# Performance work log

Hardware: AMD Instinct MI355X
Metric: run time of the kernel (lower is better)

The kernel has to match this reference:

```python
import jax, jax.numpy as jnp
import numpy as np

N, E, G = 4096, 16384, 16
IN_C, EDGE_C, H = 3, 4, 128
LN_EPS = 1e-5


def setup_inputs() -> dict:
    key = jax.random.key(0)
    ks = jax.random.split(key, 32)
    nrm = lambda k, shp, s: jax.random.normal(k, shp, jnp.float32) * s
    inp = {}
    inp["x"] = nrm(ks[0], (N, IN_C), 1.0)
    inp["edge_index"] = jax.random.randint(ks[1], (2, E), 0, N)
    inp["edge_attr"] = nrm(ks[2], (E, EDGE_C), 1.0)
    inp["batch"] = jnp.sort(jax.random.randint(ks[3], (N,), 0, G))
    inp["contingency_type"] = nrm(ks[4], (G, 4), 1.0)
    inp["load_scale"] = nrm(ks[5], (G,), 1.0)
    i = 6
    def conv_params(prefix, in_c):
        nonlocal i
        inp[prefix + "_w1"] = nrm(ks[i], (EDGE_C, 128), 1.0 / np.sqrt(EDGE_C)); i += 1
        inp[prefix + "_b1"] = jnp.zeros((128,), jnp.float32)
        inp[prefix + "_w2"] = nrm(ks[i], (128, in_c * H), 1.0 / np.sqrt(128)); i += 1
        inp[prefix + "_b2"] = jnp.zeros((in_c * H,), jnp.float32)
        inp[prefix + "_root"] = nrm(ks[i], (in_c, H), 1.0 / np.sqrt(in_c)); i += 1
        inp[prefix + "_bias"] = jnp.zeros((H,), jnp.float32)
    conv_params("c1", IN_C)
    conv_params("c2", H)
    conv_params("c3", H)
    for p in ("ln1", "ln2", "ln3"):
        inp[p + "_g"] = jnp.ones((H,), jnp.float32)
        inp[p + "_b"] = jnp.zeros((H,), jnp.float32)
    inp["lin_w"] = nrm(ks[i], (2 * H + 4 + 1, 2), 1.0 / np.sqrt(2 * H + 5)); i += 1
    inp["lin_b"] = jnp.zeros((2,), jnp.float32)
    return inp


def _nnconv(x, src, dst, edge_attr, w1, b1, w2, b2, root, bias, in_c):
    # edge MLP -> per-edge weight matrix [E, in_c, H]
    h = jax.nn.relu(edge_attr @ w1 + b1)
    W = (h @ w2 + b2).reshape(-1, in_c, H)
    msg = jnp.einsum('ei,eio->eo', x[src], W)  # gather + per-edge matmul
    s = jax.ops.segment_sum(msg, dst, num_segments=N)
    cnt = jax.ops.segment_sum(jnp.ones((msg.shape[0],), msg.dtype), dst, num_segments=N)
    agg = s / jnp.maximum(cnt, 1.0)[:, None]  # scatter-mean
    return agg + x @ root + bias


def _layernorm(x, g, b):
    m = jnp.mean(x, axis=-1, keepdims=True)
    v = jnp.mean(jnp.square(x - m), axis=-1, keepdims=True)
    return (x - m) * jax.lax.rsqrt(v + LN_EPS) * g + b


def reference(x, edge_index, edge_attr, batch, contingency_type, load_scale,
              c1_w1, c1_b1, c1_w2, c1_b2, c1_root, c1_bias,
              c2_w1, c2_b1, c2_w2, c2_b2, c2_root, c2_bias,
              c3_w1, c3_b1, c3_w2, c3_b2, c3_root, c3_bias,
              ln1_g, ln1_b, ln2_g, ln2_b, ln3_g, ln3_b,
              lin_w, lin_b):
    src, dst = edge_index[0], edge_index[1]
    h = _nnconv(x, src, dst, edge_attr, c1_w1, c1_b1, c1_w2, c1_b2, c1_root, c1_bias, IN_C)
    h = jax.nn.relu(_layernorm(h, ln1_g, ln1_b))
    h = _nnconv(h, src, dst, edge_attr, c2_w1, c2_b1, c2_w2, c2_b2, c2_root, c2_bias, H)
    h = jax.nn.elu(_layernorm(h, ln2_g, ln2_b))
    h = _nnconv(h, src, dst, edge_attr, c3_w1, c3_b1, c3_w2, c3_b2, c3_root, c3_bias, H)
    h = jax.nn.leaky_relu(_layernorm(h, ln3_g, ln3_b), negative_slope=0.01)
    # global mean / max pool over graphs
    gsum = jax.ops.segment_sum(h, batch, num_segments=G)
    gcnt = jax.ops.segment_sum(jnp.ones((N,), h.dtype), batch, num_segments=G)
    gmean = gsum / jnp.maximum(gcnt, 1.0)[:, None]
    gmax = jax.ops.segment_max(h, batch, num_segments=G)
    gmax = jnp.where(gcnt[:, None] > 0, gmax, 0.0)
    x_cat = jnp.concatenate([gmean, gmax, contingency_type, load_scale[:, None]], axis=1)
    return x_cat @ lin_w + lin_b
```

## Files before the change

### kernel.cpp

```cpp
#include <hip/hip_runtime.h>
#include <hip/hip_bf16.h>


#define N_NODES 4096
#define N_EDGES 16384
#define N_GRAPHS 16
#define HD 128
#define BM 128
#define LDB 136
#define KSPLIT 2
#define KT_PER (HD / KSPLIT)
#define SLAB_E (HD * HD)
#define PN 32

typedef unsigned short ushort_t;
typedef __attribute__((ext_vector_type(8))) short short8;
typedef __attribute__((ext_vector_type(4))) float f32x4;

static __device__ __forceinline__ ushort_t f2b(float f) {
    __hip_bfloat16 h = __float2bfloat16(f);
    union { __hip_bfloat16 h; ushort_t u; } cv; cv.h = h; return cv.u;
}
static __device__ __forceinline__ float b2f(ushort_t u) {
    union { unsigned u; float f; } cv; cv.u = ((unsigned)u) << 16; return cv.f;
}

static __device__ __forceinline__ float wave_sum(float v) {
#pragma unroll
    for (int off = 1; off < 64; off <<= 1) v += __shfl_xor(v, off, 64);
    return v;
}

__global__ __launch_bounds__(256) void count_k(const int* __restrict__ dst, float* __restrict__ cnt) {
    int e = blockIdx.x * 256 + threadIdx.x;
    atomicAdd(&cnt[dst[e]], 1.0f);
}

__global__ __launch_bounds__(128) void l1_edge(
    const float* __restrict__ x, const int* __restrict__ src, const int* __restrict__ dst,
    const float* __restrict__ ea, const float* __restrict__ w1, const float* __restrict__ b1,
    const float* __restrict__ w2, const float* __restrict__ b2, float* __restrict__ agg) {
    __shared__ float h[4][HD];
    __shared__ float xsrc[4][3];
    const int o = threadIdx.x;
    const int e0 = blockIdx.x * 4;
#pragma unroll
    for (int q = 0; q < 4; ++q) {
        float s = b1[o];
#pragma unroll
        for (int j = 0; j < 4; ++j) s = fmaf(ea[(e0 + q) * 4 + j], w1[j * HD + o], s);
        h[q][o] = fmaxf(s, 0.0f);
    }
    if (o < 12) { int q = o / 3, i = o % 3; xsrc[q][i] = x[src[e0 + q] * 3 + i]; }
    __syncthreads();
    float acc[4] = {0.f, 0.f, 0.f, 0.f};
    for (int i = 0; i < 3; ++i) {
        float bb = b2[i * HD + o];
        float w[4] = {bb, bb, bb, bb};
        for (int k = 0; k < HD; ++k) {
            float w2v = w2[k * 384 + i * HD + o];
#pragma unroll
            for (int q = 0; q < 4; ++q) w[q] = fmaf(h[q][k], w2v, w[q]);
        }
#pragma unroll
        for (int q = 0; q < 4; ++q) acc[q] = fmaf(xsrc[q][i], w[q], acc[q]);
    }
#pragma unroll
    for (int q = 0; q < 4; ++q) atomicAdd(&agg[dst[e0 + q] * HD + o], acc[q]);
}

__global__ __launch_bounds__(128) void node_update_l1(
    float* __restrict__ agg, const float* __restrict__ cnt, const float* __restrict__ x,
    const float* __restrict__ root, const float* __restrict__ bias,
    const float* __restrict__ lng, const float* __restrict__ lnb) {
    const int n = blockIdx.x, o = threadIdx.x;
    float s = bias[o];
#pragma unroll
    for (int i = 0; i < 3; ++i) s = fmaf(x[n * 3 + i], root[i * HD + o], s);
    float v = agg[n * HD + o] / fmaxf(cnt[n], 1.0f) + s;
    __shared__ float red[2];
    float ws = wave_sum(v);
    if ((o & 63) == 0) red[o >> 6] = ws;
    __syncthreads();
    float m = (red[0] + red[1]) * (1.0f / HD);
    float d = v - m;
    float ws2 = wave_sum(d * d);
    __syncthreads();
    if ((o & 63) == 0) red[o >> 6] = ws2;
    __syncthreads();
    float var = (red[0] + red[1]) * (1.0f / HD);
    float y = d * rsqrtf(var + 1e-5f) * lng[o] + lnb[o];
    agg[n * HD + o] = fmaxf(y, 0.0f);
}

__global__ __launch_bounds__(256) void w2t_prep(const float* __restrict__ w2,
                                                const float* __restrict__ b2,
                                                ushort_t* __restrict__ w2t) {
    __shared__ ushort_t tile[HD][LDB];
    const int kt = blockIdx.x;
    const int t = threadIdx.x;
    const float* srcp = (kt < HD) ? (w2 + kt * HD * HD) : b2;
    for (int c = 0; c < 64; ++c) {
        int flat = c * 256 + t;
        int i = flat >> 7, o = flat & 127;
        tile[o][i] = f2b(srcp[i * HD + o]);
    }
    __syncthreads();
    uint4* outp = (uint4*)(w2t + (size_t)kt * SLAB_E);
    for (int it = 0; it < 8; ++it) {
        int c = it * 256 + t;
        int ng = c >> 9, j = (c >> 6) & 7, l = c & 63;
        int ni = j >> 2, kb = j & 3;
        int R  = ng * 32 + ni * 16 + (l & 15);
        int ke = kb * 32 + (l >> 4) * 8;
        outp[c] = *(const uint4*)&tile[R][ke];
    }
}

__global__ __launch_bounds__(512, 2) void gemm_mfma(
    const float* __restrict__ hprev, const float* __restrict__ ea,
    const float* __restrict__ w1, const float* __restrict__ b1,
    const ushort_t* __restrict__ w2t,
    const int* __restrict__ src, const int* __restrict__ dst,
    float* __restrict__ agg) {
    __shared__ ushort_t Xs[SLAB_E];
    __shared__ ushort_t HeT[KT_PER][BM];

    const int t = threadIdx.x;
    const int lane = t & 63, quad = lane >> 4, l16 = lane & 15;
    const int wave = t >> 6;
    const int mg = wave >> 2;
    const int ng = wave & 3;
    const int eb = blockIdx.x >> 1;
    const int ks = blockIdx.x & 1;
    const int k0 = ks * KT_PER;
    const int e0 = eb * BM;
    const int rbase = mg * 64;

    {
        const int le = t >> 2;
        const int j0 = (t & 3) * 4;
        const int r7 = le & 7;
        const float* rp = hprev + src[e0 + le] * HD + (t & 3) * 32;
        ushort_t* xrow = Xs + le * HD;
#pragma unroll
        for (int c = 0; c < 4; ++c) {
            float4 va = ((const float4*)rp)[2 * c];
            float4 vb = ((const float4*)rp)[2 * c + 1];
            uint4 pk;
            pk.x = (unsigned)f2b(va.x) | ((unsigned)f2b(va.y) << 16);
            pk.y = (unsigned)f2b(va.z) | ((unsigned)f2b(va.w) << 16);
            pk.z = (unsigned)f2b(vb.x) | ((unsigned)f2b(vb.y) << 16);
            pk.w = (unsigned)f2b(vb.z) | ((unsigned)f2b(vb.w) << 16);
            *(uint4*)&xrow[((j0 + c) ^ r7) << 3] = pk;
        }
    }

    {
        const int e = t & 127;
        const float4 av = ((const float4*)ea)[e0 + e];
        for (int kl = t >> 7; kl < KT_PER; kl += 4) {
            const int kt = k0 + kl;
            float s = b1[kt];
            s = fmaf(av.x, w1[0 * HD + kt], s);
            s = fmaf(av.y, w1[1 * HD + kt], s);
            s = fmaf(av.z, w1[2 * HD + kt], s);
            s = fmaf(av.w, w1[3 * HD + kt], s);
            HeT[kl][e] = f2b(fmaxf(s, 0.0f));
        }
    }
    __syncthreads();

    short8 afrag[4][4];
#pragma unroll
    for (int mi = 0; mi < 4; ++mi) {
        const int R = rbase + mi * 16 + l16;
        const ushort_t* rowp = Xs + R * HD;
        const int r7 = R & 7;
#pragma unroll
        for (int kb = 0; kb < 4; ++kb)
            afrag[mi][kb] = *(const short8*)&rowp[((kb * 4 + quad) ^ r7) << 3];
    }

    f32x4 acc[4][2];
#pragma unroll
    for (int mi = 0; mi < 4; ++mi)
#pragma unroll
        for (int ni = 0; ni < 2; ++ni)
            acc[mi][ni] = (f32x4){0.f, 0.f, 0.f, 0.f};

    const ushort_t* bbase = w2t + (size_t)ng * 4096 + (size_t)lane * 8;

#define LOADB(bf, slab)                                                         \
    {                                                                           \
        const ushort_t* bw = bbase + (size_t)(slab) * SLAB_E;                   \
        _Pragma("unroll") for (int ni = 0; ni < 2; ++ni)                        \
            _Pragma("unroll") for (int kb = 0; kb < 4; ++kb)                    \
                bf[ni][kb] = *(const short8*)(bw + (ni * 4 + kb) * 512);        \
    }
#define CONSUME(bf, s)                                                          \
    {                                                                           \
        _Pragma("unroll") for (int mi = 0; mi < 4; ++mi) {                      \
            ushort4 hv = *(const ushort4*)&HeT[s][rbase + mi * 16 + quad * 4];  \
            float h0 = b2f(hv.x), h1 = b2f(hv.y), h2 = b2f(hv.z), h3 = b2f(hv.w);\
            _Pragma("unroll") for (int ni = 0; ni < 2; ++ni) {                  \
                f32x4 p = {0.f, 0.f, 0.f, 0.f};                                 \
                _Pragma("unroll") for (int kb = 0; kb < 4; ++kb)                \
                    p = __builtin_amdgcn_mfma_f32_16x16x32_bf16(                \
                        afrag[mi][kb], bf[ni][kb], p, 0, 0, 0);                 \
                acc[mi][ni][0] = fmaf(h0, p[0], acc[mi][ni][0]);                \
                acc[mi][ni][1] = fmaf(h1, p[1], acc[mi][ni][1]);                \
                acc[mi][ni][2] = fmaf(h2, p[2], acc[mi][ni][2]);                \
                acc[mi][ni][3] = fmaf(h3, p[3], acc[mi][ni][3]);                \
            }                                                                   \
        }                                                                       \
    }

    short8 bfA[2][4], bfB[2][4];
    LOADB(bfA, k0);
    for (int s = 0; s < KT_PER; s += 2) {
        LOADB(bfB, k0 + s + 1);
        CONSUME(bfA, s);
        __builtin_amdgcn_s_barrier();
        if (s + 2 < KT_PER) LOADB(bfA, k0 + s + 2)
        else if (ks == 1)   LOADB(bfA, HD);
        CONSUME(bfB, s + 1);
        __builtin_amdgcn_s_barrier();
    }
    if (ks == 1) {
#pragma unroll
        for (int mi = 0; mi < 4; ++mi)
#pragma unroll
            for (int ni = 0; ni < 2; ++ni) {
                f32x4 p = {0.f, 0.f, 0.f, 0.f};
#pragma unroll
                for (int kb = 0; kb < 4; ++kb)
                    p = __builtin_amdgcn_mfma_f32_16x16x32_bf16(
                        afrag[mi][kb], bfA[ni][kb], p, 0, 0, 0);
                acc[mi][ni][0] += p[0]; acc[mi][ni][1] += p[1];
                acc[mi][ni][2] += p[2]; acc[mi][ni][3] += p[3];
            }
    }
#undef LOADB
#undef CONSUME

#pragma unroll
    for (int mi = 0; mi < 4; ++mi) {
#pragma unroll
        for (int r = 0; r < 4; ++r) {
            const int dn = dst[e0 + rbase + mi * 16 + quad * 4 + r];
#pragma unroll
            for (int ni = 0; ni < 2; ++ni)
                atomicAdd(&agg[dn * HD + ng * 32 + ni * 16 + l16], acc[mi][ni][r]);
        }
    }
}

__global__ __launch_bounds__(128) void node_update(
    float* __restrict__ agg, const float* __restrict__ cnt,
    const float* __restrict__ hprev, const float* __restrict__ root, const float* __restrict__ bias,
    const float* __restrict__ lng, const float* __restrict__ lnb, int act) {
    const int n = blockIdx.x, o = threadIdx.x;
    __shared__ float hr[HD];
    hr[o] = hprev[n * HD + o];
    __syncthreads();
    float s = bias[o];
#pragma unroll 8
    for (int k = 0; k < HD; ++k) s = fmaf(hr[k], root[k * HD + o], s);
    float v = agg[n * HD + o] / fmaxf(cnt[n], 1.0f) + s;
    __shared__ float red[2];
    float ws = wave_sum(v);
    if ((o & 63) == 0) red[o >> 6] = ws;
    __syncthreads();
    float m = (red[0] + red[1]) * (1.0f / HD);
    float d = v - m;
    float ws2 = wave_sum(d * d);
    __syncthreads();
    if ((o & 63) == 0) red[o >> 6] = ws2;
    __syncthreads();
    float var = (red[0] + red[1]) * (1.0f / HD);
    float y = d * rsqrtf(var + 1e-5f) * lng[o] + lnb[o];
    if (act == 1) y = (y > 0.0f) ? y : expm1f(y);
    else y = (y > 0.0f) ? y : 0.01f * y;
    agg[n * HD + o] = y;
}

static __device__ __forceinline__ unsigned fkey(float f) {
    unsigned b = __float_as_uint(f);
    return (b & 0x80000000u) ? ~b : (b | 0x80000000u);
}
__global__ __launch_bounds__(128) void pool_scatter(
    const float* __restrict__ h3, const int* __restrict__ batch,
    float* __restrict__ gsum, unsigned* __restrict__ gmaxk, int* __restrict__ gcnt) {
    const int o = threadIdx.x;
    const int nb = blockIdx.x * PN;
    float sum = 0.0f, mx = -3.0e38f;
    int gcur = batch[nb];
    int run = 0;
    for (int j = 0; j < PN; ++j) {
        const int n = nb + j;
        const int g = batch[n];
        const float v = h3[n * HD + o];
        if (g != gcur) {
            atomicAdd(&gsum[gcur * HD + o], sum);
            atomicMax(&gmaxk[gcur * HD + o], fkey(mx));
            if (o == 0) atomicAdd(&gcnt[gcur], run);
            sum = 0.0f; mx = -3.0e38f; run = 0; gcur = g;
        }
        sum += v; mx = fmaxf(mx, v); ++run;
    }
    atomicAdd(&gsum[gcur * HD + o], sum);
    atomicMax(&gmaxk[gcur * HD + o], fkey(mx));
    if (o == 0) atomicAdd(&gcnt[gcur], run);
}

__global__ __launch_bounds__(128) void pool_head2(
    const float* __restrict__ gsum, const unsigned* __restrict__ gmaxk, const int* __restrict__ gcnt,
    const float* __restrict__ cont, const float* __restrict__ ls,
    const float* __restrict__ lin_w, const float* __restrict__ lin_b, float* __restrict__ out) {
    const int g = blockIdx.x, o = threadIdx.x;
    const int c = gcnt[g];
    __shared__ float xcat[2 * HD + 5];
    xcat[o] = gsum[g * HD + o] / fmaxf((float)c, 1.0f);
    unsigned key = gmaxk[g * HD + o];
    unsigned bits = (key & 0x80000000u) ? (key & 0x7FFFFFFFu) : ~key;
    xcat[HD + o] = (c > 0) ? __uint_as_float(bits) : 0.0f;
    if (o < 4) xcat[2 * HD + o] = cont[g * 4 + o];
    if (o == 0) xcat[2 * HD + 4] = ls[g];
    __syncthreads();
    if (o < 2) {
        float r = lin_b[o];
        for (int ri = 0; ri < 2 * HD + 5; ++ri) r = fmaf(xcat[ri], lin_w[ri * 2 + o], r);
        out[g * 2 + o] = r;
    }
}

extern "C" void kernel_launch(void* const* d_in, const int* in_sizes, int n_in,
                              void* d_out, int out_size, void* d_ws, size_t ws_size,
                              hipStream_t stream) {
    const float* x     = (const float*)d_in[0];
    const int*   ei    = (const int*)d_in[1];
    const float* ea    = (const float*)d_in[2];
    const int*   batch = (const int*)d_in[3];
    const float* cont  = (const float*)d_in[4];
    const float* ls    = (const float*)d_in[5];
    const float *c1_w1 = (const float*)d_in[6],  *c1_b1 = (const float*)d_in[7];
    const float *c1_w2 = (const float*)d_in[8],  *c1_b2 = (const float*)d_in[9];
    const float *c1_rt = (const float*)d_in[10], *c1_bs = (const float*)d_in[11];
    const float *c2_w1 = (const float*)d_in[12], *c2_b1 = (const float*)d_in[13];
    const float *c2_w2 = (const float*)d_in[14], *c2_b2 = (const float*)d_in[15];
    const float *c2_rt = (const float*)d_in[16], *c2_bs = (const float*)d_in[17];
    const float *c3_w1 = (const float*)d_in[18], *c3_b1 = (const float*)d_in[19];
    const float *c3_w2 = (const float*)d_in[20], *c3_b2 = (const float*)d_in[21];
    const float *c3_rt = (const float*)d_in[22], *c3_bs = (const float*)d_in[23];
    const float *ln1g = (const float*)d_in[24], *ln1b = (const float*)d_in[25];
    const float *ln2g = (const float*)d_in[26], *ln2b = (const float*)d_in[27];
    const float *ln3g = (const float*)d_in[28], *ln3b = (const float*)d_in[29];
    const float *lin_w = (const float*)d_in[30], *lin_b = (const float*)d_in[31];
    float* out = (float*)d_out;

    float*    cnt  = (float*)d_ws;
    float*    bufA = cnt + N_NODES;
    float*    bufB = bufA + N_NODES * HD;
    ushort_t* w2t  = (ushort_t*)(bufB + N_NODES * HD);
    float*    gsum = (float*)(w2t + (HD + 1) * HD * HD);
    unsigned* gmaxk = (unsigned*)(gsum + N_GRAPHS * HD);
    int*      gcnt = (int*)(gmaxk + N_GRAPHS * HD);
    const int* src = ei;
    const int* dst = ei + N_EDGES;

    hipMemsetAsync(cnt, 0, N_NODES * sizeof(float), stream);
    count_k<<<N_EDGES / 256, 256, 0, stream>>>(dst, cnt);

    hipMemsetAsync(bufA, 0, N_NODES * HD * sizeof(float), stream);
    l1_edge<<<N_EDGES / 4, 128, 0, stream>>>(x, src, dst, ea, c1_w1, c1_b1, c1_w2, c1_b2, bufA);
    node_update_l1<<<N_NODES, 128, 0, stream>>>(bufA, cnt, x, c1_rt, c1_bs, ln1g, ln1b);

    w2t_prep<<<HD + 1, 256, 0, stream>>>(c2_w2, c2_b2, w2t);
    hipMemsetAsync(bufB, 0, N_NODES * HD * sizeof(float), stream);
    gemm_mfma<<<(N_EDGES / BM) * KSPLIT, 512, 0, stream>>>(bufA, ea, c2_w1, c2_b1, w2t, src, dst, bufB);
    node_update<<<N_NODES, 128, 0, stream>>>(bufB, cnt, bufA, c2_rt, c2_bs, ln2g, ln2b, 1);

    w2t_prep<<<HD + 1, 256, 0, stream>>>(c3_w2, c3_b2, w2t);
    hipMemsetAsync(bufA, 0, N_NODES * HD * sizeof(float), stream);
    gemm_mfma<<<(N_EDGES / BM) * KSPLIT, 512, 0, stream>>>(bufB, ea, c3_w1, c3_b1, w2t, src, dst, bufA);
    node_update<<<N_NODES, 128, 0, stream>>>(bufA, cnt, bufB, c3_rt, c3_bs, ln3g, ln3b, 2);

    hipMemsetAsync(gsum, 0, (2 * N_GRAPHS * HD + N_GRAPHS) * sizeof(float), stream);
    pool_scatter<<<N_NODES / PN, 128, 0, stream>>>(bufA, batch, gsum, gmaxk, gcnt);
    pool_head2<<<N_GRAPHS, 128, 0, stream>>>(gsum, gmaxk, gcnt, cont, ls, lin_w, lin_b, out);
}
```

Baseline: 386.2 us.

## Rewrite layer-1 NNConv edge kernel as bf16 MFMA GEMM with hoisted bias

Replaces the scalar per-edge FP32 loop of the first NNConv with a block-tiled bf16 MFMA kernel. The edge-MLP hidden activations go into swizzled shared memory and multiply a pre-transposed bf16 copy of w2. The result is scaled by the source features and scattered with atomics. The b2 bias term moves to the node update by accumulating the per-destination sum of source features in the counting kernel. This cuts the large FP32 FMA cost of layer 1, at the cost of bf16 precision for the edge weights and extra atomics.

```diff
diff --git a/kernel.cpp b/kernel.cpp
--- a/kernel.cpp
+++ b/kernel.cpp
@@ -31,53 +31,170 @@
     return v;
 }
 
-__global__ __launch_bounds__(256) void count_k(const int* __restrict__ dst, float* __restrict__ cnt) {
+__global__ __launch_bounds__(256) void count_feat(
+    const int* __restrict__ src, const int* __restrict__ dst, const float* __restrict__ x,
+    float* __restrict__ cnt, float* __restrict__ sfeat) {
     int e = blockIdx.x * 256 + threadIdx.x;
-    atomicAdd(&cnt[dst[e]], 1.0f);
-}
-
-__global__ __launch_bounds__(128) void l1_edge(
+    int d = dst[e], s = src[e];
+    atomicAdd(&cnt[d], 1.0f);
+    atomicAdd(&sfeat[d * 4 + 0], x[s * 3 + 0]);
+    atomicAdd(&sfeat[d * 4 + 1], x[s * 3 + 1]);
+    atomicAdd(&sfeat[d * 4 + 2], x[s * 3 + 2]);
+}
+
+__global__ __launch_bounds__(256) void w2r_prep(const float* __restrict__ w2,
+                                                ushort_t* __restrict__ w2r) {
+    __shared__ ushort_t tile[HD][LDB];
+    const int i = blockIdx.x;
+    const int t = threadIdx.x;
+    for (int c = 0; c < 64; ++c) {
+        int flat = c * 256 + t;
+        int k = flat >> 7, o = flat & 127;
+        tile[o][k] = f2b(w2[k * 384 + i * HD + o]);
+    }
+    __syncthreads();
+    uint4* outp = (uint4*)(w2r + (size_t)i * SLAB_E);
+    for (int it = 0; it < 8; ++it) {
+        int c = it * 256 + t;
+        int ng = c >> 9, j = (c >> 6) & 7, l = c & 63;
+        int ni = j >> 2, kb = j & 3;
+        int R  = ng * 32 + ni * 16 + (l & 15);
+        int ke = kb * 32 + (l >> 4) * 8;
+        outp[c] = *(const uint4*)&tile[R][ke];
+    }
+}
+
+__global__ __launch_bounds__(512, 2) void l1_gemm(
     const float* __restrict__ x, const int* __restrict__ src, const int* __restrict__ dst,
     const float* __restrict__ ea, const float* __restrict__ w1, const float* __restrict__ b1,
-    const float* __restrict__ w2, const float* __restrict__ b2, float* __restrict__ agg) {
-    __shared__ float h[4][HD];
-    __shared__ float xsrc[4][3];
-    const int o = threadIdx.x;
-    const int e0 = blockIdx.x * 4;
-#pragma unroll
-    for (int q = 0; q < 4; ++q) {
-        float s = b1[o];
-#pragma unroll
-        for (int j = 0; j < 4; ++j) s = fmaf(ea[(e0 + q) * 4 + j], w1[j * HD + o], s);
-        h[q][o] = fmaxf(s, 0.0f);
-    }
-    if (o < 12) { int q = o / 3, i = o % 3; xsrc[q][i] = x[src[e0 + q] * 3 + i]; }
-    __syncthreads();
-    float acc[4] = {0.f, 0.f, 0.f, 0.f};
-    for (int i = 0; i < 3; ++i) {
-        float bb = b2[i * HD + o];
-        float w[4] = {bb, bb, bb, bb};
-        for (int k = 0; k < HD; ++k) {
-            float w2v = w2[k * 384 + i * HD + o];
-#pragma unroll
-            for (int q = 0; q < 4; ++q) w[q] = fmaf(h[q][k], w2v, w[q]);
-        }
-#pragma unroll
-        for (int q = 0; q < 4; ++q) acc[q] = fmaf(xsrc[q][i], w[q], acc[q]);
-    }
-#pragma unroll
-    for (int q = 0; q < 4; ++q) atomicAdd(&agg[dst[e0 + q] * HD + o], acc[q]);
+    const ushort_t* __restrict__ w2r, float* __restrict__ agg) {
+    __shared__ ushort_t Hs[SLAB_E];
+    __shared__ float    XV[3][BM];
+
+    const int t = threadIdx.x;
+    const int lane = t & 63, quad = lane >> 4, l16 = lane & 15;
+    const int wave = t >> 6;
+    const int mg = wave >> 2;
+    const int ng = wave & 3;
+    const int e0 = blockIdx.x * BM;
+    const int rbase = mg * 64;
+
+    {
+        const int e = t & 127;
+        const int kb32 = (t >> 7) * 32;
+        const float4 av = ((const float4*)ea)[e0 + e];
+        if (t < 128) {
+            const int n = src[e0 + t];
+            XV[0][t] = x[n * 3 + 0]; XV[1][t] = x[n * 3 + 1]; XV[2][t] = x[n * 3 + 2];
+        }
+        const int r7 = e & 7;
+        ushort_t* hrow = Hs + e * HD;
+#pragma unroll
+        for (int c = 0; c < 4; ++c) {
+            const int kbase = kb32 + c * 8;
+            unsigned pk0, pk1, pk2, pk3;
+#pragma unroll
+            for (int u = 0; u < 4; ++u) {
+                const int ka = kbase + 2 * u, kb = ka + 1;
+                float s0 = b1[ka];
+                s0 = fmaf(av.x, w1[0 * HD + ka], s0);
+                s0 = fmaf(av.y, w1[1 * HD + ka], s0);
+                s0 = fmaf(av.z, w1[2 * HD + ka], s0);
+                s0 = fmaf(av.w, w1[3 * HD + ka], s0);
+                float s1 = b1[kb];
+                s1 = fmaf(av.x, w1[0 * HD + kb], s1);
+                s1 = fmaf(av.y, w1[1 * HD + kb], s1);
+                s1 = fmaf(av.z, w1[2 * HD + kb], s1);
+                s1 = fmaf(av.w, w1[3 * HD + kb], s1);
+                unsigned pr = (unsigned)f2b(fmaxf(s0, 0.0f)) |
+                              ((unsigned)f2b(fmaxf(s1, 0.0f)) << 16);
+                if (u == 0) pk0 = pr; else if (u == 1) pk1 = pr;
+                else if (u == 2) pk2 = pr; else pk3 = pr;
+            }
+            uint4 v; v.x = pk0; v.y = pk1; v.z = pk2; v.w = pk3;
+            *(uint4*)&hrow[(((kbase >> 3) ^ r7) << 3)] = v;
+        }
+    }
+    __syncthreads();
+
+    short8 afrag[4][4];
+#pragma unroll
+    for (int mi = 0; mi < 4; ++mi) {
+        const int R = rbase + mi * 16 + l16;
+        const ushort_t* rowp = Hs + R * HD;
+        const int r7 = R & 7;
+#pragma unroll
+        for (int kb = 0; kb < 4; ++kb)
+            afrag[mi][kb] = *(const short8*)&rowp[((kb * 4 + quad) ^ r7) << 3];
+    }
+
+    f32x4 acc[4][2];
+#pragma unroll
+    for (int mi = 0; mi < 4; ++mi)
+#pragma unroll
+        for (int ni = 0; ni < 2; ++ni)
+            acc[mi][ni] = (f32x4){0.f, 0.f, 0.f, 0.f};
+
+    const ushort_t* bbase = w2r + (size_t)ng * 4096 + (size_t)lane * 8;
+
+#define LOADB(bf, slab)                                                         \
+    {                                                                           \
+        const ushort_t* bw = bbase + (size_t)(slab) * SLAB_E;                   \
+        _Pragma("unroll") for (int ni = 0; ni < 2; ++ni)                        \
+            _Pragma("unroll") for (int kb = 0; kb < 4; ++kb)                    \
+                bf[ni][kb] = *(const short8*)(bw + (ni * 4 + kb) * 512);        \
+    }
+#define CONSUME_XV(bf, i)                                                       \
+    {                                                                           \
+        _Pragma("unroll") for (int mi = 0; mi < 4; ++mi) {                      \
+            float4 xv = *(const float4*)&XV[i][rbase + mi * 16 + quad * 4];     \
+            _Pragma("unroll") for (int ni = 0; ni < 2; ++ni) {                  \
+                f32x4 p = {0.f, 0.f, 0.f, 0.f};                                 \
+                _Pragma("unroll") for (int kb = 0; kb < 4; ++kb)                \
+                    p = __builtin_amdgcn_mfma_f32_16x16x32_bf16(                \
+                        afrag[mi][kb], bf[ni][kb], p, 0, 0, 0);                 \
+                acc[mi][ni][0] = fmaf(xv.x, p[0], acc[mi][ni][0]);              \
+                acc[mi][ni][1] = fmaf(xv.y, p[1], acc[mi][ni][1]);              \
+                acc[mi][ni][2] = fmaf(xv.z, p[2], acc[mi][ni][2]);              \
+                acc[mi][ni][3] = fmaf(xv.w, p[3], acc[mi][ni][3]);              \
+            }                                                                   \
+        }                                                                       \
+    }
+
+    short8 bfA[2][4], bfB[2][4];
+    LOADB(bfA, 0);
+    LOADB(bfB, 1);
+    CONSUME_XV(bfA, 0);
+    LOADB(bfA, 2);
+    CONSUME_XV(bfB, 1);
+    CONSUME_XV(bfA, 2);
+#undef LOADB
+#undef CONSUME_XV
+
+#pragma unroll
+    for (int mi = 0; mi < 4; ++mi) {
+#pragma unroll
+        for (int r = 0; r < 4; ++r) {
+            const int dn = dst[e0 + rbase + mi * 16 + quad * 4 + r];
+#pragma unroll
+            for (int ni = 0; ni < 2; ++ni)
+                atomicAdd(&agg[dn * HD + ng * 32 + ni * 16 + l16], acc[mi][ni][r]);
+        }
+    }
 }
 
 __global__ __launch_bounds__(128) void node_update_l1(
-    float* __restrict__ agg, const float* __restrict__ cnt, const float* __restrict__ x,
-    const float* __restrict__ root, const float* __restrict__ bias,
-    const float* __restrict__ lng, const float* __restrict__ lnb) {
+    float* __restrict__ agg, const float* __restrict__ cnt, const float* __restrict__ sfeat,
+    const float* __restrict__ x, const float* __restrict__ root, const float* __restrict__ bias,
+    const float* __restrict__ b2, const float* __restrict__ lng, const float* __restrict__ lnb) {
     const int n = blockIdx.x, o = threadIdx.x;
     float s = bias[o];
 #pragma unroll
     for (int i = 0; i < 3; ++i) s = fmaf(x[n * 3 + i], root[i * HD + o], s);
-    float v = agg[n * HD + o] / fmaxf(cnt[n], 1.0f) + s;
+    float sb = 0.0f;
+#pragma unroll
+    for (int i = 0; i < 3; ++i) sb = fmaf(sfeat[n * 4 + i], b2[i * HD + o], sb);
+    float v = (agg[n * HD + o] + sb) / fmaxf(cnt[n], 1.0f) + s;
     __shared__ float red[2];
     float ws = wave_sum(v);
     if ((o & 63) == 0) red[o >> 6] = ws;
@@ -359,22 +476,24 @@
     const float *lin_w = (const float*)d_in[30], *lin_b = (const float*)d_in[31];
     float* out = (float*)d_out;
 
-    float*    cnt  = (float*)d_ws;
-    float*    bufA = cnt + N_NODES;
-    float*    bufB = bufA + N_NODES * HD;
-    ushort_t* w2t  = (ushort_t*)(bufB + N_NODES * HD);
-    float*    gsum = (float*)(w2t + (HD + 1) * HD * HD);
+    float*    cnt   = (float*)d_ws;
+    float*    sfeat = cnt + N_NODES;
+    float*    bufA  = sfeat + 4 * N_NODES;
+    float*    bufB  = bufA + N_NODES * HD;
+    ushort_t* w2t   = (ushort_t*)(bufB + N_NODES * HD);
+    float*    gsum  = (float*)(w2t + (HD + 1) * HD * HD);
     unsigned* gmaxk = (unsigned*)(gsum + N_GRAPHS * HD);
-    int*      gcnt = (int*)(gmaxk + N_GRAPHS * HD);
+    int*      gcnt  = (int*)(gmaxk + N_GRAPHS * HD);
     const int* src = ei;
     const int* dst = ei + N_EDGES;
 
-    hipMemsetAsync(cnt, 0, N_NODES * sizeof(float), stream);
-    count_k<<<N_EDGES / 256, 256, 0, stream>>>(dst, cnt);
-
+    hipMemsetAsync(cnt, 0, 5 * N_NODES * sizeof(float), stream);
+    count_feat<<<N_EDGES / 256, 256, 0, stream>>>(src, dst, x, cnt, sfeat);
+
+    w2r_prep<<<3, 256, 0, stream>>>(c1_w2, w2t);
     hipMemsetAsync(bufA, 0, N_NODES * HD * sizeof(float), stream);
-    l1_edge<<<N_EDGES / 4, 128, 0, stream>>>(x, src, dst, ea, c1_w1, c1_b1, c1_w2, c1_b2, bufA);
-    node_update_l1<<<N_NODES, 128, 0, stream>>>(bufA, cnt, x, c1_rt, c1_bs, ln1g, ln1b);
+    l1_gemm<<<N_EDGES / BM, 512, 0, stream>>>(x, src, dst, ea, c1_w1, c1_b1, w2t, bufA);
+    node_update_l1<<<N_NODES, 128, 0, stream>>>(bufA, cnt, sfeat, x, c1_rt, c1_bs, c1_b2, ln1g, ln1b);
 
     w2t_prep<<<HD + 1, 256, 0, stream>>>(c2_w2, c2_b2, w2t);
     hipMemsetAsync(bufB, 0, N_NODES * HD * sizeof(float), stream);
```

Result: faster. 368.8 us (-4.5%).
